# Performance work log

Measured on AMD Instinct MI355X. Metric: run time of the kernel, lower is better.

## Reference

```python
import jax, jax.numpy as jnp
import numpy as np

B, L, H, V = 256, 200, 128, 50000
NLAYER, K = 2, 20
NEG = -1e10


def setup_inputs() -> dict:
    key = jax.random.key(0)
    ks = jax.random.split(key, 14)
    lens = jax.random.randint(ks[0], (B,), 50, L + 1)
    pos = jnp.arange(L)
    valid = pos[None, :] < lens[:, None]                       # [B,L] bool
    seq = jnp.where(valid, jax.random.randint(ks[1], (B, L), 1, V), 0)
    lengths = valid.astype(jnp.int32)                          # >0 where real token
    reverse_lengths = jnp.where(valid, lens[:, None] - pos[None, :], 0)  # 1..len, 0=pad

    def nrm(k, shape, s=0.02):
        return jax.random.normal(k, shape, jnp.float32) * s

    emb_w = nrm(ks[2], (V, H)).at[0].set(0.0)
    wnoise_w = nrm(ks[3], (L + 1, H)).at[0].set(0.0)
    cluster_w = nrm(ks[4], (L + 1, 1)).at[0].set(0.0)
    ffn1_w = nrm(ks[5], (H, H), 0.05)
    ffn1_b = jnp.zeros((H,), jnp.float32)
    ffn2_w = nrm(ks[6], (H, H), 0.05)
    ffn2_b = jnp.zeros((H,), jnp.float32)
    ln_g = jnp.ones((H,), jnp.float32)
    ln_b = jnp.zeros((H,), jnp.float32)
    gate_w = nrm(ks[7], (2 * H, H), 0.05)
    coff = jax.random.normal(ks[8], (NLAYER, B, L, L), jnp.float32)  # fixed noise (torch.normal)
    return dict(seq=seq, lengths=lengths, reverse_lengths=reverse_lengths,
                emb_w=emb_w, wnoise_w=wnoise_w, cluster_w=cluster_w,
                ffn1_w=ffn1_w, ffn1_b=ffn1_b, ffn2_w=ffn2_w, ffn2_b=ffn2_b,
                ln_g=ln_g, ln_b=ln_b, gate_w=gate_w, coff=coff)


def _sp(x):  # torch.nn.Softplus(threshold=1): identity above 1
    return jnp.where(x > 1.0, x, jnp.log1p(jnp.exp(jnp.minimum(x, 1.0))))


def _forward(seq, lengths, reverse_lengths, emb_w, wnoise_w, cluster_w,
             ffn1_w, ffn1_b, ffn2_w, ffn2_b, ln_g, ln_b, gate_w, coff):
    b, l = seq.shape
    mask = (lengths > 0).astype(jnp.float32)                   # [B,L]
    hidden = emb_w[seq]                                        # [B,L,H]
    slen = jnp.sum(mask, axis=1)                               # [B]
    e_s = hidden[jnp.arange(b), (slen - 1).astype(jnp.int32)]  # last real token state
    zero_layer = jnp.sum(hidden, 1) / slen[:, None]
    layer_collect = [zero_layer]
    eye = jnp.eye(l, dtype=hidden.dtype)
    pair_ok = mask[:, :, None] * mask[:, None, :]              # [B,L,L]
    for i in range(coff.shape[0]):
        wn = wnoise_w[reverse_lengths]                         # [B,L,H]
        sim = jnp.einsum('bld,bmd->blm', hidden, hidden)
        nrm = jnp.linalg.norm(hidden, axis=2, keepdims=True)   # [B,L,1]
        sim = sim / (nrm * nrm.transpose(0, 2, 1) + 1e-6)      # cosine similarity
        diag = cluster_w[reverse_lengths][..., 0]              # [B,L]
        sim = sim + diag[:, :, None] * eye                     # diag_embed add
        sim = sim + coff[i] * _sp(jnp.einsum('bld,bmd->blm', hidden, wn))
        msim = jnp.where(pair_ok == 0.0, NEG, sim)             # masked_fill
        _, idx = jax.lax.top_k(msim, K)                        # [B,L,K]
        sel = jnp.zeros_like(msim).at[jnp.arange(b)[:, None, None],
                                      jnp.arange(l)[None, :, None], idx].set(1.0)
        edges = sel * (msim > NEG).astype(msim.dtype)          # top-k & above-threshold
        cluster_label = edges.transpose(0, 2, 1)
        sim_softmax = jax.nn.softmax(msim, axis=2)
        ssm = cluster_label * sim_softmax                      # [B,L,L] sparse-weighted
        update_hidden = jnp.einsum('blm,bmd->bld', ssm, hidden)
        cmask = jnp.sum(ssm, axis=2)                           # [B,L]
        cmask = cmask / jnp.maximum(jnp.linalg.norm(cmask, axis=1, keepdims=True), 1e-12)
        if i > 0:
            update_hidden = update_hidden * (slen > 1.0).astype(hidden.dtype)[:, None, None]
        feed1 = jax.nn.relu(update_hidden @ ffn1_w + ffn1_b)
        pre = feed1 @ ffn2_w + ffn2_b + update_hidden          # dropout = identity (eval)
        mu = jnp.mean(pre, -1, keepdims=True)
        var = jnp.var(pre, -1, keepdims=True)
        feed2 = (pre - mu) / jnp.sqrt(var + 1e-5) * ln_g + ln_b
        layer_collect.append(jnp.sum(feed2 * cmask[:, :, None], 1))
    e_c = jnp.mean(jnp.stack(layer_collect, 1), 1)             # [B,H]
    alpha = jax.nn.sigmoid(jnp.concatenate([e_c, e_s], -1) @ gate_w)
    sess = alpha * e_c + (1.0 - alpha) * e_s
    scores = sess @ emb_w.T                                    # [B,V]
    return scores


def reference(seq, lengths, reverse_lengths, emb_w, wnoise_w, cluster_w,
              ffn1_w, ffn1_b, ffn2_w, ffn2_b, ln_g, ln_b, gate_w, coff):
    scores = _forward(seq, lengths, reverse_lengths, emb_w, wnoise_w, cluster_w,
                      ffn1_w, ffn1_b, ffn2_w, ffn2_b, ln_g, ln_b, gate_w, coff)
    return (scores, jnp.asarray(0.0, jnp.float32))  # con_loss == 0 when abs=True
```

## Files before the change

kernel.cpp:

```cpp
#include <hip/hip_runtime.h>
#include <cstdint>
#include <cstddef>

namespace {
constexpr int B = 256, L = 200, H = 128, V = 50000, TK = 20;
constexpr int NT = 1563;
constexpr float NEGV = -1e10f;
}

using bf16x8 = __attribute__((ext_vector_type(8))) short;
using s16x8  = __attribute__((ext_vector_type(8))) short;
using f32x16 = __attribute__((ext_vector_type(16))) float;

__device__ inline unsigned short f2bf(float f) {
  unsigned int u = __float_as_uint(f);
  unsigned int r = (u + 0x7fffu + ((u >> 16) & 1u)) >> 16;
  return (unsigned short)r;
}

#define DPP_QUAD_XOR1 0xB1
#define DPP_QUAD_XOR2 0x4E
#define DPP_ROW_HMIRR 0x141
#define DPP_ROW_MIRR  0x140

template <int CTRL>
__device__ inline unsigned dpp16_max_step(unsigned v) {
  unsigned t = (unsigned)__builtin_amdgcn_update_dpp(0, (int)v, CTRL, 0xF, 0xF, true);
  return v > t ? v : t;
}
__device__ inline unsigned grp16_max(unsigned v) {
  v = dpp16_max_step<DPP_QUAD_XOR1>(v);
  v = dpp16_max_step<DPP_QUAD_XOR2>(v);
  v = dpp16_max_step<DPP_ROW_HMIRR>(v);
  v = dpp16_max_step<DPP_ROW_MIRR>(v);
  return v;
}
template <int CTRL>
__device__ inline float dpp16_add_step(float v) {
  int t = __builtin_amdgcn_update_dpp(0, __float_as_int(v), CTRL, 0xF, 0xF, true);
  return v + __int_as_float(t);
}
__device__ inline float grp16_sum(float v) {
  v = dpp16_add_step<DPP_QUAD_XOR1>(v);
  v = dpp16_add_step<DPP_QUAD_XOR2>(v);
  v = dpp16_add_step<DPP_ROW_HMIRR>(v);
  v = dpp16_add_step<DPP_ROW_MIRR>(v);
  return v;
}

__device__ inline unsigned f2key(float f) {
  unsigned b = __float_as_uint(f);
  unsigned m = (unsigned)((int)b >> 31);
  return b ^ (m | 0x80000000u);
}
__device__ inline float key2f(unsigned u) {
  unsigned b = (u & 0x80000000u) ? (u & 0x7fffffffu) : ~u;
  return __uint_as_float(b);
}

__global__ __launch_bounds__(256) void k_embed(const int* __restrict__ seq,
                                               const int* __restrict__ rev,
                                               const float* __restrict__ emb,
                                               const float* __restrict__ wnoise,
                                               float* __restrict__ hidden,
                                               float* __restrict__ nrm,
                                               s16x8* __restrict__ hbh,
                                               s16x8* __restrict__ hbl,
                                               s16x8* __restrict__ wnh,
                                               s16x8* __restrict__ wnl) {
  int b = blockIdx.x / 7, lt = blockIdx.x % 7;
  int t = threadIdx.x;
  int r = t >> 3, c2 = t & 7;
  int l = lt * 32 + r;
  bool valid = l < L;
  float vv[16], wv[16];
  if (valid) {
    int row = b * L + l;
    int tok = seq[row];
    const float4* ep = (const float4*)&emb[(size_t)tok * H + c2 * 16];
    const float4* wp = (const float4*)&wnoise[(size_t)rev[row] * H + c2 * 16];
#pragma unroll
    for (int i = 0; i < 4; ++i) {
      float4 x = ep[i];
      vv[i * 4 + 0] = x.x; vv[i * 4 + 1] = x.y; vv[i * 4 + 2] = x.z; vv[i * 4 + 3] = x.w;
      float4 y = wp[i];
      wv[i * 4 + 0] = y.x; wv[i * 4 + 1] = y.y; wv[i * 4 + 2] = y.z; wv[i * 4 + 3] = y.w;
    }
  } else {
#pragma unroll
    for (int i = 0; i < 16; ++i) { vv[i] = 0.f; wv[i] = 0.f; }
  }
  if (valid) {
    int row = b * L + l;
#pragma unroll
    for (int i = 0; i < 4; ++i)
      *(float4*)&hidden[(size_t)row * H + c2 * 16 + i * 4] =
          make_float4(vv[i * 4], vv[i * 4 + 1], vv[i * 4 + 2], vv[i * 4 + 3]);
    float s = 0.f;
#pragma unroll
    for (int i = 0; i < 16; ++i) s += vv[i] * vv[i];
    s += __shfl_down(s, 4, 8);
    s += __shfl_down(s, 2, 8);
    s += __shfl_down(s, 1, 8);
    if (c2 == 0) nrm[row] = sqrtf(s);
  }
  s16x8 h0, h1, l0, l1, w0, w1, x0, x1;
#pragma unroll
  for (int i = 0; i < 8; ++i) {
    unsigned short hi = f2bf(vv[i]);
    h0[i] = (short)hi;
    l0[i] = (short)f2bf(vv[i] - __uint_as_float((unsigned)hi << 16));
    unsigned short wh = f2bf(wv[i]);
    w0[i] = (short)wh;
    x0[i] = (short)f2bf(wv[i] - __uint_as_float((unsigned)wh << 16));
  }
#pragma unroll
  for (int i = 0; i < 8; ++i) {
    unsigned short hi = f2bf(vv[8 + i]);
    h1[i] = (short)hi;
    l1[i] = (short)f2bf(vv[8 + i] - __uint_as_float((unsigned)hi << 16));
    unsigned short wh = f2bf(wv[8 + i]);
    w1[i] = (short)wh;
    x1[i] = (short)f2bf(wv[8 + i] - __uint_as_float((unsigned)wh << 16));
  }
  size_t fi0 = ((size_t)(b * 7 + lt) * 8 + c2) * 64 + r;
  size_t fi1 = fi0 + 32;
  hbh[fi0] = h0; hbh[fi1] = h1;
  hbl[fi0] = l0; hbl[fi1] = l1;
  wnh[fi0] = w0; wnh[fi1] = w1;
  wnl[fi0] = x0; wnl[fi1] = x1;
}

__global__ __launch_bounds__(512) void k_init(const int* __restrict__ lengths,
                                              const float* __restrict__ hidden,
                                              float* __restrict__ ecacc,
                                              float* __restrict__ e_s) {
  int b = blockIdx.x, tid = threadIdx.x;
  __shared__ float part[4][128];
  __shared__ int wcnt[8];
  __shared__ int s_slen;
  int c = (tid < L && lengths[b * L + tid] > 0) ? 1 : 0;
  for (int o = 32; o > 0; o >>= 1) c += __shfl_down(c, o, 64);
  if ((tid & 63) == 0) wcnt[tid >> 6] = c;
  __syncthreads();
  if (tid == 0) {
    int s = 0;
#pragma unroll
    for (int i = 0; i < 8; ++i) s += wcnt[i];
    s_slen = s;
  }
  int h = tid & 127, seg = tid >> 7;
  float s = 0.f;
  for (int l = seg; l < L; l += 4) s += hidden[(size_t)(b * L + l) * H + h];
  part[seg][h] = s;
  __syncthreads();
  if (tid < 128) {
    float tot = part[0][h] + part[1][h] + part[2][h] + part[3][h];
    int slen = s_slen;
    ecacc[b * H + h] = tot / (float)slen;
    e_s[b * H + h] = hidden[(size_t)(b * L + slen - 1) * H + h];
  }
}

__global__ __launch_bounds__(256) void k_simws(const s16x8* __restrict__ hbh,
                                               const s16x8* __restrict__ hbl,
                                               const s16x8* __restrict__ wnh,
                                               const s16x8* __restrict__ wnl,
                                               const float* __restrict__ nrm,
                                               const int* __restrict__ rev,
                                               const float* __restrict__ cluster,
                                               float* __restrict__ S0,
                                               float* __restrict__ WS) {
  int orig = blockIdx.x;
  int xcd = orig & 7, slot = orig >> 3;
  int b = xcd * 32 + slot / 14;
  int rem = slot % 14;
  int lt = rem >> 1, half = rem & 1;
  int wid = threadIdx.x >> 6, lane = threadIdx.x & 63;
  int mt = half * 4 + wid;
  if (mt > 6) return;
  int lr = lane & 31, kh = lane >> 5;
  size_t abase = ((size_t)(b * 7 + lt) * 8) * 64 + lane;
  bf16x8 ah[8], al[8];
#pragma unroll
  for (int ks = 0; ks < 8; ++ks) {
    ah[ks] = (bf16x8)hbh[abase + ks * 64];
    al[ks] = (bf16x8)hbl[abase + ks * 64];
  }
  size_t bbase = ((size_t)(b * 7 + mt) * 8) * 64 + lane;
  f32x16 accs = {}, accw = {};
#pragma unroll
  for (int ks = 0; ks < 8; ++ks) {
    bf16x8 bhh = (bf16x8)hbh[bbase + ks * 64];
    bf16x8 bhl = (bf16x8)hbl[bbase + ks * 64];
    bf16x8 bwh = (bf16x8)wnh[bbase + ks * 64];
    bf16x8 bwl = (bf16x8)wnl[bbase + ks * 64];
    accs = __builtin_amdgcn_mfma_f32_32x32x16_bf16(ah[ks], bhh, accs, 0, 0, 0);
    accs = __builtin_amdgcn_mfma_f32_32x32x16_bf16(ah[ks], bhl, accs, 0, 0, 0);
    accs = __builtin_amdgcn_mfma_f32_32x32x16_bf16(al[ks], bhh, accs, 0, 0, 0);
    accw = __builtin_amdgcn_mfma_f32_32x32x16_bf16(ah[ks], bwh, accw, 0, 0, 0);
    accw = __builtin_amdgcn_mfma_f32_32x32x16_bf16(ah[ks], bwl, accw, 0, 0, 0);
    accw = __builtin_amdgcn_mfma_f32_32x32x16_bf16(al[ks], bwh, accw, 0, 0, 0);
  }
  int m = mt * 32 + lr;
  if (m < L) {
    float nm = nrm[b * L + m];
#pragma unroll
    for (int r = 0; r < 16; ++r) {
      int row = lt * 32 + (r & 3) + 8 * (r >> 2) + 4 * kh;
      if (row < L) {
        float nl = nrm[b * L + row];
        float s0 = accs[r] * __builtin_amdgcn_rcpf(nl * nm + 1e-6f);
        if (row == m) s0 += cluster[rev[b * L + row]];
        size_t o = (size_t)(b * L + row) * L + m;
        S0[o] = s0;
        float x = accw[r];
        WS[o] = (x > 1.f) ? x : __logf(1.f + __expf(x));
      }
    }
  }
}

__global__ __launch_bounds__(256) void k_rowpass(const float* __restrict__ S0,
                                                 const float* __restrict__ WS,
                                                 const float* __restrict__ coff_i,
                                                 const int* __restrict__ lengths,
                                                 float* __restrict__ P,
                                                 unsigned char* __restrict__ ET) {
  int wid = threadIdx.x >> 6, lane = threadIdx.x & 63;
  int g = lane >> 4, q = lane & 15;
  int bb = blockIdx.x / 13, blk = blockIdx.x % 13;
  int l = blk * 16 + wid * 4 + g;
  bool lvalid = l < L;
  int lrow = bb * L + (lvalid ? l : 0);
  bool mask_l = lvalid && (lengths[lrow] > 0);
  size_t base = (size_t)lrow * L;
  float val[13]; unsigned key[13]; unsigned vmask = 0;
#pragma unroll
  for (int j = 0; j < 13; ++j) {
    int m = q + 16 * j;
    float v = 0.f; bool ok = false;
    if (mask_l && m < L) {
      ok = lengths[bb * L + m] > 0;
      if (ok) v = S0[base + m] + coff_i[base + m] * WS[base + m];
    }
    val[j] = v;
    key[j] = ok ? f2key(v) : 0u;
    vmask |= ok ? (1u << j) : 0u;
  }
  unsigned Mu = 0u;
  for (int t = 0; t < TK; ++t) {
    unsigned lv = key[0]; int lj = 0;
#pragma unroll
    for (int j = 1; j < 13; ++j) {
      bool gt = key[j] > lv;
      lv = gt ? key[j] : lv;
      lj = gt ? j : lj;
    }
    unsigned gm = grp16_max(lv);
    if (t == 0) Mu = gm;
    if (__all(gm == 0u)) break;
    unsigned long long bal = __ballot(lv == gm && gm != 0u);
    unsigned long long mine = bal & (0xFFFFull << (g * 16));
    int owner = mine ? (int)__builtin_ctzll(mine) : -1;
    bool is_owner = (lane == owner);
    if (is_owner) {
      int m = q + 16 * lj;
      ET[((size_t)bb * L + m) * L + l] = 1;
    }
#pragma unroll
    for (int j = 0; j < 13; ++j) key[j] = (is_owner && lj == j) ? 0u : key[j];
  }
  float M = key2f(Mu);
  float e[13]; float s = 0.f;
#pragma unroll
  for (int j = 0; j < 13; ++j) {
    float ev = ((vmask >> j) & 1u) ? __expf(val[j] - M) : 0.f;
    e[j] = ev; s += ev;
  }
  s = grp16_sum(s);
  float inv = (s > 0.f) ? __builtin_amdgcn_rcpf(s) : 0.f;
  if (lvalid) {
#pragma unroll
    for (int j = 0; j < 13; ++j) {
      int m = q + 16 * j;
      if (m < L) P[base + m] = e[j] * inv;
    }
  }
}

__global__ __launch_bounds__(256) void k_compact(float* __restrict__ P,
                                                 unsigned char* __restrict__ ET,
                                                 float* __restrict__ cmask,
                                                 int* __restrict__ cnt) {
  int wid = threadIdx.x >> 6, lane = threadIdx.x & 63;
  int row = blockIdx.x * 4 + wid;
  size_t base = (size_t)row * L;
  float w[4];
  float s = 0.f;
#pragma unroll
  for (int j = 0; j < 4; ++j) {
    int m = lane + 64 * j;
    float ww = 0.f;
    if (m < L) ww = P[base + m] * (float)ET[base + m];
    w[j] = ww; s += ww;
  }
  float ssum = s;
  for (int off = 1; off < 64; off <<= 1) ssum += __shfl_xor(ssum, off, 64);
  if (lane == 0) cmask[row] = ssum;
  int pos_base = 0;
#pragma unroll
  for (int j = 0; j < 4; ++j) {
    bool nz = (w[j] != 0.f);
    unsigned long long mk = __ballot(nz);
    int rank = __popcll(mk & ((1ull << lane) - 1ull));
    if (nz) {
      int pos = pos_base + rank;
      ET[base + pos] = (unsigned char)(lane + 64 * j);
      P[base + pos] = w[j];
    }
    pos_base += (int)__popcll(mk);
  }
  if (lane == 0) cnt[row] = pos_base;
}

__global__ __launch_bounds__(64) void k_cnorm(float* __restrict__ cmask) {
  int b = blockIdx.x, lane = threadIdx.x;
  float v[4]; float s = 0.f;
#pragma unroll
  for (int j = 0; j < 4; ++j) {
    int l = lane + 64 * j;
    float x = (l < L) ? cmask[b * L + l] : 0.f;
    v[j] = x; s += x * x;
  }
  for (int off = 1; off < 64; off <<= 1) s += __shfl_xor(s, off, 64);
  float inv = 1.f / fmaxf(sqrtf(s), 1e-12f);
#pragma unroll
  for (int j = 0; j < 4; ++j) {
    int l = lane + 64 * j;
    if (l < L) cmask[b * L + l] = v[j] * inv;
  }
}

__global__ __launch_bounds__(256) void k_update(const float* __restrict__ P,
                                                const unsigned char* __restrict__ ET,
                                                const int* __restrict__ cnt,
                                                const float* __restrict__ hidden,
                                                float* __restrict__ upd) {
  int row = blockIdx.x * 2 + (threadIdx.x >> 7);
  int h = threadIdx.x & 127;
  int b = row / L;
  size_t base = (size_t)row * L;
  int n = cnt[row];
  float acc = 0.f;
  for (int e0 = 0; e0 < n; e0 += TK) {
    float w[TK]; int m[TK];
    float4 p4[5];
#pragma unroll
    for (int i = 0; i < 5; ++i) p4[i] = *(const float4*)&P[base + e0 + i * 4];
#pragma unroll
    for (int i = 0; i < 5; ++i) {
      w[i * 4 + 0] = p4[i].x; w[i * 4 + 1] = p4[i].y;
      w[i * 4 + 2] = p4[i].z; w[i * 4 + 3] = p4[i].w;
    }
#pragma unroll
    for (int e = 0; e < TK; ++e) m[e] = ET[base + e0 + e];
    float hv[TK];
#pragma unroll
    for (int e = 0; e < TK; ++e)
      hv[e] = hidden[(size_t)(b * L + m[e]) * H + h];
#pragma unroll
    for (int e = 0; e < TK; ++e)
      acc += ((e0 + e) < n ? w[e] : 0.f) * hv[e];
  }
  upd[(size_t)row * H + h] = acc;
}

__global__ __launch_bounds__(256) void k_ffn(float* __restrict__ upd,
                                             const float* __restrict__ W1,
                                             const float* __restrict__ b1,
                                             const float* __restrict__ W2,
                                             const float* __restrict__ b2,
                                             const float* __restrict__ g,
                                             const float* __restrict__ beta,
                                             const float* __restrict__ cmask) {
  constexpr int AS = 136;
  __shared__ __align__(16) char smem[4 * 64 * AS * 2];
  short* ahs = (short*)smem;
  short* als = ahs + 64 * AS;
  short* f1h = (short*)(smem + 2 * 64 * AS * 2);
  short* f1l = f1h + 64 * AS;
  float (*ps)[132] = (float (*)[132])smem;
  __shared__ float mus[64], rsd[64];
  int row0 = blockIdx.x * 64;
  int tid = threadIdx.x;
  int wid = tid >> 6, lane = tid & 63;
  int lr = lane & 31, kh = lane >> 5;
  int n0 = wid * 32;
  int n = n0 + lr;
#pragma unroll
  for (int it = 0; it < 8; ++it) {
    int f = it * 256 + tid;
    int r = f >> 5, c4 = (f & 31) * 4;
    float4 v = *(const float4*)&upd[(size_t)(row0 + r) * H + c4];
    float vv[4] = {v.x, v.y, v.z, v.w};
    unsigned short hh[4]; short ll[4];
#pragma unroll
    for (int q2 = 0; q2 < 4; ++q2) {
      hh[q2] = f2bf(vv[q2]);
      ll[q2] = (short)f2bf(vv[q2] - __uint_as_float((unsigned)hh[q2] << 16));
    }
    uint2 ph = make_uint2((unsigned)hh[0] | ((unsigned)hh[1] << 16),
                          (unsigned)hh[2] | ((unsigned)hh[3] << 16));
    uint2 pl = make_uint2((unsigned short)ll[0] | ((unsigned)(unsigned short)ll[1] << 16),
                          (unsigned short)ll[2] | ((unsigned)(unsigned short)ll[3] << 16));
    *(uint2*)&ahs[r * AS + c4] = ph;
    *(uint2*)&als[r * AS + c4] = pl;
  }
  __syncthreads();
  bf16x8 wfh[8], wfl[8];
#pragma unroll
  for (int ks = 0; ks < 8; ++ks) {
#pragma unroll
    for (int i = 0; i < 8; ++i) {
      float w = W1[(size_t)(ks * 16 + kh * 8 + i) * H + n];
      unsigned short hi = f2bf(w);
      wfh[ks][i] = (short)hi;
      wfl[ks][i] = (short)f2bf(w - __uint_as_float((unsigned)hi << 16));
    }
  }
  f32x16 acc0, acc1;
  {
    float bv = b1[n];
#pragma unroll
    for (int r = 0; r < 16; ++r) { acc0[r] = bv; acc1[r] = bv; }
  }
#pragma unroll
  for (int ks = 0; ks < 8; ++ks) {
    bf16x8 xh0 = *(const bf16x8*)&ahs[(0 * 32 + lr) * AS + ks * 16 + kh * 8];
    bf16x8 xl0 = *(const bf16x8*)&als[(0 * 32 + lr) * AS + ks * 16 + kh * 8];
    bf16x8 xh1 = *(const bf16x8*)&ahs[(1 * 32 + lr) * AS + ks * 16 + kh * 8];
    bf16x8 xl1 = *(const bf16x8*)&als[(1 * 32 + lr) * AS + ks * 16 + kh * 8];
    acc0 = __builtin_amdgcn_mfma_f32_32x32x16_bf16(xh0, wfh[ks], acc0, 0, 0, 0);
    acc0 = __builtin_amdgcn_mfma_f32_32x32x16_bf16(xl0, wfh[ks], acc0, 0, 0, 0);
    acc0 = __builtin_amdgcn_mfma_f32_32x32x16_bf16(xh0, wfl[ks], acc0, 0, 0, 0);
    acc1 = __builtin_amdgcn_mfma_f32_32x32x16_bf16(xh1, wfh[ks], acc1, 0, 0, 0);
    acc1 = __builtin_amdgcn_mfma_f32_32x32x16_bf16(xl1, wfh[ks], acc1, 0, 0, 0);
    acc1 = __builtin_amdgcn_mfma_f32_32x32x16_bf16(xh1, wfl[ks], acc1, 0, 0, 0);
  }
#pragma unroll
  for (int r = 0; r < 16; ++r) {
    int crow = (r & 3) + 8 * (r >> 2) + 4 * kh;
    float f0 = fmaxf(acc0[r], 0.f);
    unsigned short h0 = f2bf(f0);
    f1h[crow * AS + n] = (short)h0;
    f1l[crow * AS + n] = (short)f2bf(f0 - __uint_as_float((unsigned)h0 << 16));
    float f1v = fmaxf(acc1[r], 0.f);
    unsigned short h1 = f2bf(f1v);
    f1h[(32 + crow) * AS + n] = (short)h1;
    f1l[(32 + crow) * AS + n] = (short)f2bf(f1v - __uint_as_float((unsigned)h1 << 16));
  }
  __syncthreads();
#pragma unroll
  for (int ks = 0; ks < 8; ++ks) {
#pragma unroll
    for (int i = 0; i < 8; ++i) {
      float w = W2[(size_t)(ks * 16 + kh * 8 + i) * H + n];
      unsigned short hi = f2bf(w);
      wfh[ks][i] = (short)hi;
      wfl[ks][i] = (short)f2bf(w - __uint_as_float((unsigned)hi << 16));
    }
  }
  {
    float bv = b2[n];
#pragma unroll
    for (int r = 0; r < 16; ++r) { acc0[r] = bv; acc1[r] = bv; }
  }
#pragma unroll
  for (int ks = 0; ks < 8; ++ks) {
    bf16x8 xh0 = *(const bf16x8*)&f1h[(0 * 32 + lr) * AS + ks * 16 + kh * 8];
    bf16x8 xl0 = *(const bf16x8*)&f1l[(0 * 32 + lr) * AS + ks * 16 + kh * 8];
    bf16x8 xh1 = *(const bf16x8*)&f1h[(1 * 32 + lr) * AS + ks * 16 + kh * 8];
    bf16x8 xl1 = *(const bf16x8*)&f1l[(1 * 32 + lr) * AS + ks * 16 + kh * 8];
    acc0 = __builtin_amdgcn_mfma_f32_32x32x16_bf16(xh0, wfh[ks], acc0, 0, 0, 0);
    acc0 = __builtin_amdgcn_mfma_f32_32x32x16_bf16(xl0, wfh[ks], acc0, 0, 0, 0);
    acc0 = __builtin_amdgcn_mfma_f32_32x32x16_bf16(xh0, wfl[ks], acc0, 0, 0, 0);
    acc1 = __builtin_amdgcn_mfma_f32_32x32x16_bf16(xh1, wfh[ks], acc1, 0, 0, 0);
    acc1 = __builtin_amdgcn_mfma_f32_32x32x16_bf16(xl1, wfh[ks], acc1, 0, 0, 0);
    acc1 = __builtin_amdgcn_mfma_f32_32x32x16_bf16(xh1, wfl[ks], acc1, 0, 0, 0);
  }
#pragma unroll
  for (int r = 0; r < 16; ++r) {
    int crow = (r & 3) + 8 * (r >> 2) + 4 * kh;
    float p0 = acc0[r] + upd[(size_t)(row0 + crow) * H + n];
    float p1 = acc1[r] + upd[(size_t)(row0 + 32 + crow) * H + n];
    acc0[r] = p0; acc1[r] = p1;
    ps[crow][n] = p0;
    ps[32 + crow][n] = p1;
  }
  __syncthreads();
  {
    int r = tid >> 2, sub = tid & 3;
    float s = 0.f, sq = 0.f;
#pragma unroll
    for (int j = 0; j < 8; ++j) {
      float4 x = *(const float4*)&ps[r][sub * 32 + j * 4];
      s += x.x + x.y + x.z + x.w;
      sq += x.x * x.x + x.y * x.y + x.z * x.z + x.w * x.w;
    }
    s += __shfl_down(s, 2, 4);  s += __shfl_down(s, 1, 4);
    sq += __shfl_down(sq, 2, 4); sq += __shfl_down(sq, 1, 4);
    if (sub == 0) {
      float mu = s * (1.f / 128.f);
      float var = sq * (1.f / 128.f) - mu * mu;
      mus[r] = mu;
      rsd[r] = rsqrtf(var + 1e-5f);
    }
  }
  __syncthreads();
  {
    float gn = g[n], bn = beta[n];
#pragma unroll
    for (int r = 0; r < 16; ++r) {
      int crow = (r & 3) + 8 * (r >> 2) + 4 * kh;
      float o0 = ((acc0[r] - mus[crow]) * rsd[crow] * gn + bn) * cmask[row0 + crow];
      float o1 = ((acc1[r] - mus[32 + crow]) * rsd[32 + crow] * gn + bn) * cmask[row0 + 32 + crow];
      upd[(size_t)(row0 + crow) * H + n] = o0;
      upd[(size_t)(row0 + 32 + crow) * H + n] = o1;
    }
  }
}

__global__ __launch_bounds__(512) void k_ecadd(const float* __restrict__ wf,
                                               float* __restrict__ ecacc) {
  int b = blockIdx.x, tid = threadIdx.x;
  __shared__ float part[4][128];
  int h = tid & 127, seg = tid >> 7;
  float s = 0.f;
  for (int l = seg; l < L; l += 4) s += wf[(size_t)(b * L + l) * H + h];
  part[seg][h] = s;
  __syncthreads();
  if (tid < 128)
    ecacc[b * H + h] += part[0][h] + part[1][h] + part[2][h] + part[3][h];
}

__global__ __launch_bounds__(256) void k_embconv(const float* __restrict__ emb,
                                                 s16x8* __restrict__ ebh,
                                                 s16x8* __restrict__ ebl) {
  int nt = blockIdx.x;
  int t = threadIdx.x;
  int r = t >> 3, c2 = t & 7;
  int n = nt * 32 + r;
  float vv[16];
  if (n < V) {
    const float4* ep = (const float4*)&emb[(size_t)n * H + c2 * 16];
#pragma unroll
    for (int i = 0; i < 4; ++i) {
      float4 x = ep[i];
      vv[i * 4 + 0] = x.x; vv[i * 4 + 1] = x.y; vv[i * 4 + 2] = x.z; vv[i * 4 + 3] = x.w;
    }
  } else {
#pragma unroll
    for (int i = 0; i < 16; ++i) vv[i] = 0.f;
  }
  s16x8 h0, h1, l0, l1;
#pragma unroll
  for (int i = 0; i < 8; ++i) {
    unsigned short hi = f2bf(vv[i]);
    h0[i] = (short)hi;
    l0[i] = (short)f2bf(vv[i] - __uint_as_float((unsigned)hi << 16));
    unsigned short hj = f2bf(vv[8 + i]);
    h1[i] = (short)hj;
    l1[i] = (short)f2bf(vv[8 + i] - __uint_as_float((unsigned)hj << 16));
  }
  size_t fi0 = ((size_t)nt * 8 + c2) * 64 + r;
  size_t fi1 = fi0 + 32;
  ebh[fi0] = h0; ebh[fi1] = h1;
  ebl[fi0] = l0; ebl[fi1] = l1;
}

__global__ __launch_bounds__(128) void k_gate(const float* __restrict__ ecacc,
                                              const float* __restrict__ e_s,
                                              const float* __restrict__ gw,
                                              float* __restrict__ sess,
                                              float* __restrict__ out) {
  __shared__ float cat[256];
  int b = blockIdx.x, h = threadIdx.x;
  float ec = ecacc[b * H + h] * (1.f / 3.f);
  float es = e_s[b * H + h];
  cat[h] = ec; cat[128 + h] = es;
  __syncthreads();
  float a = 0.f;
  for (int j = 0; j < 256; ++j) a = fmaf(cat[j], gw[(size_t)j * H + h], a);
  a = 1.f / (1.f + __expf(-a));
  sess[b * H + h] = a * ec + (1.f - a) * es;
  if (b == 0 && h == 0) out[(size_t)B * V] = 0.f;
}

__global__ __launch_bounds__(256) void k_scores(const float* __restrict__ sess,
                                                const s16x8* __restrict__ ebh,
                                                const s16x8* __restrict__ ebl,
                                                float* __restrict__ out) {
  int wid = threadIdx.x >> 6, lane = threadIdx.x & 63;
  int lr = lane & 31, kh = lane >> 5;
  int mt = blockIdx.y;
  int m = mt * 32 + lr;
  bf16x8 ah[8], al[8];
#pragma unroll
  for (int ks = 0; ks < 8; ++ks) {
    const float* sp = &sess[(size_t)m * H + ks * 16 + kh * 8];
    float4 a = *(const float4*)sp;
    float4 c = *(const float4*)(sp + 4);
    float av[8] = {a.x, a.y, a.z, a.w, c.x, c.y, c.z, c.w};
#pragma unroll
    for (int i = 0; i < 8; ++i) {
      unsigned short hi = f2bf(av[i]);
      ah[ks][i] = (short)hi;
      al[ks][i] = (short)f2bf(av[i] - __uint_as_float((unsigned)hi << 16));
    }
  }
  int ntEnd = min(blockIdx.x * 16 + 16, NT);
  for (int nt = blockIdx.x * 16 + wid; nt < ntEnd; nt += 4) {
    size_t bbase = ((size_t)nt * 8) * 64 + lane;
    f32x16 acc = {};
#pragma unroll
    for (int ks = 0; ks < 8; ++ks) {
      bf16x8 bh = (bf16x8)ebh[bbase + ks * 64];
      bf16x8 bl = (bf16x8)ebl[bbase + ks * 64];
      acc = __builtin_amdgcn_mfma_f32_32x32x16_bf16(ah[ks], bh, acc, 0, 0, 0);
      acc = __builtin_amdgcn_mfma_f32_32x32x16_bf16(al[ks], bh, acc, 0, 0, 0);
      acc = __builtin_amdgcn_mfma_f32_32x32x16_bf16(ah[ks], bl, acc, 0, 0, 0);
    }
    int n = nt * 32 + lr;
    if (n < V) {
#pragma unroll
      for (int r = 0; r < 16; ++r) {
        int row = mt * 32 + (r & 3) + 8 * (r >> 2) + 4 * kh;
        out[(size_t)row * V + n] = acc[r];
      }
    }
  }
}

extern "C" void kernel_launch(void* const* d_in, const int* in_sizes, int n_in,
                              void* d_out, int out_size, void* d_ws, size_t ws_size,
                              hipStream_t stream) {
  const int*   seq  = (const int*)d_in[0];
  const int*   lens = (const int*)d_in[1];
  const int*   rev  = (const int*)d_in[2];
  const float* emb  = (const float*)d_in[3];
  const float* wnz  = (const float*)d_in[4];
  const float* clw  = (const float*)d_in[5];
  const float* w1   = (const float*)d_in[6];
  const float* fb1  = (const float*)d_in[7];
  const float* w2   = (const float*)d_in[8];
  const float* fb2  = (const float*)d_in[9];
  const float* lng  = (const float*)d_in[10];
  const float* lnb  = (const float*)d_in[11];
  const float* gw   = (const float*)d_in[12];
  const float* coff = (const float*)d_in[13];
  float* out = (float*)d_out;

  char* ws = (char*)d_ws;
  size_t off = 0;
  auto alloc = [&](size_t bytes) {
    void* p = ws + off;
    off += (bytes + 255) & ~(size_t)255;
    return p;
  };
  float* hidden = (float*)alloc((size_t)B * L * H * 4);
  float* nrm    = (float*)alloc((size_t)B * L * 4);
  float* S0     = (float*)alloc((size_t)B * L * L * 4);
  float* WS     = (float*)alloc((size_t)B * L * L * 4);
  float* P      = (float*)alloc((size_t)B * L * L * 4);
  float* upd    = (float*)alloc((size_t)B * L * H * 4);
  float* cmask  = (float*)alloc((size_t)B * L * 4);
  int*   cnt    = (int*)alloc((size_t)B * L * 4);
  float* e_s    = (float*)alloc((size_t)B * H * 4);
  float* ecacc  = (float*)alloc((size_t)B * H * 4);
  float* sess   = (float*)alloc((size_t)B * H * 4);
  unsigned char* ET = (unsigned char*)alloc((size_t)B * L * L);
  s16x8* hbh = (s16x8*)alloc((size_t)B * 7 * 8 * 64 * 16);
  s16x8* wnh = (s16x8*)alloc((size_t)B * 7 * 8 * 64 * 16);
  s16x8* hbl = (s16x8*)P;
  s16x8* wnl = (s16x8*)upd;
  s16x8* ebh = (s16x8*)S0;
  s16x8* ebl = (s16x8*)WS;

  k_embed<<<B * 7, 256, 0, stream>>>(seq, rev, emb, wnz, hidden, nrm,
                                     hbh, hbl, wnh, wnl);
  k_init<<<B, 512, 0, stream>>>(lens, hidden, ecacc, e_s);
  k_simws<<<B * 14, 256, 0, stream>>>(hbh, hbl, wnh, wnl, nrm, rev, clw, S0, WS);

  for (int i = 0; i < 2; ++i) {
    hipMemsetAsync(ET, 0, (size_t)B * L * L, stream);
    k_rowpass<<<B * 13, 256, 0, stream>>>(S0, WS, coff + (size_t)i * B * L * L,
                                          lens, P, ET);
    k_compact<<<B * L / 4, 256, 0, stream>>>(P, ET, cmask, cnt);
    k_cnorm<<<B, 64, 0, stream>>>(cmask);
    k_update<<<B * L / 2, 256, 0, stream>>>(P, ET, cnt, hidden, upd);
    k_ffn<<<B * L / 64, 256, 0, stream>>>(upd, w1, fb1, w2, fb2, lng, lnb, cmask);
    k_ecadd<<<B, 512, 0, stream>>>(upd, ecacc);
  }

  k_embconv<<<NT, 256, 0, stream>>>(emb, ebh, ebl);
  k_gate<<<B, 128, 0, stream>>>(ecacc, e_s, gw, sess, out);
  k_scores<<<dim3((NT + 15) / 16, 8), 256, 0, stream>>>(sess, ebh, ebl, out);
}
```

Baseline: 460.0 us.

## Fuse compact and update into a gather kernel; two rows per group in rowpass top-k

The row-pass kernel now handles two query rows per 16-lane group. It keeps a running top-3 per lane plus an LDS copy of the keys, so most top-k iterations no longer rescan all 13 registers. The separate compact and update kernels are merged into one k_gather kernel. It compacts the selected weights and indices into shared memory and then gathers hidden rows, which avoids writing and re-reading the compacted P and ET arrays and saves a launch. The cost is more LDS use in rowpass (27 words per thread), and the two-row layout roughly halves the grid size.

```diff
diff --git a/kernel.cpp b/kernel.cpp
--- a/kernel.cpp
+++ b/kernel.cpp
@@ -227,101 +227,179 @@
                                                  const int* __restrict__ lengths,
                                                  float* __restrict__ P,
                                                  unsigned char* __restrict__ ET) {
+  __shared__ unsigned klds[256 * 27];
   int wid = threadIdx.x >> 6, lane = threadIdx.x & 63;
   int g = lane >> 4, q = lane & 15;
-  int bb = blockIdx.x / 13, blk = blockIdx.x % 13;
-  int l = blk * 16 + wid * 4 + g;
-  bool lvalid = l < L;
-  int lrow = bb * L + (lvalid ? l : 0);
-  bool mask_l = lvalid && (lengths[lrow] > 0);
-  size_t base = (size_t)lrow * L;
-  float val[13]; unsigned key[13]; unsigned vmask = 0;
+  int bb = blockIdx.x / 7, blk = blockIdx.x % 7;
+  int g16 = wid * 4 + g;
+  int lA = blk * 32 + g16 * 2, lB = lA + 1;
+  bool lvA = lA < L, lvB = lB < L;
+  int lrowA = bb * L + (lvA ? lA : 0);
+  int lrowB = bb * L + (lvB ? lB : 0);
+  bool mA = lvA && (lengths[lrowA] > 0);
+  bool mB = lvB && (lengths[lrowB] > 0);
+  size_t baseA = (size_t)lrowA * L, baseB = (size_t)lrowB * L;
+  int kbA = threadIdx.x * 27, kbB = kbA + 13;
+  float valA[13], valB[13]; unsigned vmA = 0, vmB = 0;
+  unsigned a0 = 0, a1 = 0, a2 = 0; int aj0 = 0, aj1 = 0, aj2 = 0;
+  unsigned c0 = 0, c1 = 0, c2 = 0; int cj0 = 0, cj1 = 0, cj2 = 0;
 #pragma unroll
   for (int j = 0; j < 13; ++j) {
     int m = q + 16 * j;
-    float v = 0.f; bool ok = false;
-    if (mask_l && m < L) {
-      ok = lengths[bb * L + m] > 0;
-      if (ok) v = S0[base + m] + coff_i[base + m] * WS[base + m];
-    }
-    val[j] = v;
-    key[j] = ok ? f2key(v) : 0u;
-    vmask |= ok ? (1u << j) : 0u;
-  }
-  unsigned Mu = 0u;
+    bool colOk = (m < L) && (lengths[bb * L + m] > 0);
+    bool okA = mA && colOk, okB = mB && colOk;
+    float vA = 0.f, vB = 0.f;
+    if (okA) vA = S0[baseA + m] + coff_i[baseA + m] * WS[baseA + m];
+    if (okB) vB = S0[baseB + m] + coff_i[baseB + m] * WS[baseB + m];
+    valA[j] = vA; valB[j] = vB;
+    unsigned kA = okA ? f2key(vA) : 0u;
+    unsigned kB = okB ? f2key(vB) : 0u;
+    vmA |= okA ? (1u << j) : 0u;
+    vmB |= okB ? (1u << j) : 0u;
+    klds[kbA + j] = kA;
+    klds[kbB + j] = kB;
+    if (kA > a0)      { a2 = a1; aj2 = aj1; a1 = a0; aj1 = aj0; a0 = kA; aj0 = j; }
+    else if (kA > a1) { a2 = a1; aj2 = aj1; a1 = kA; aj1 = j; }
+    else if (kA > a2) { a2 = kA; aj2 = j; }
+    if (kB > c0)      { c2 = c1; cj2 = cj1; c1 = c0; cj1 = cj0; c0 = kB; cj0 = j; }
+    else if (kB > c1) { c2 = c1; cj2 = cj1; c1 = kB; cj1 = j; }
+    else if (kB > c2) { c2 = kB; cj2 = j; }
+  }
+  unsigned ccA = a0; int cjA = aj0; int consA = 0;
+  unsigned ccB = c0; int cjB = cj0; int consB = 0;
+  unsigned MuA = 0u, MuB = 0u;
   for (int t = 0; t < TK; ++t) {
-    unsigned lv = key[0]; int lj = 0;
-#pragma unroll
-    for (int j = 1; j < 13; ++j) {
-      bool gt = key[j] > lv;
-      lv = gt ? key[j] : lv;
-      lj = gt ? j : lj;
-    }
-    unsigned gm = grp16_max(lv);
-    if (t == 0) Mu = gm;
-    if (__all(gm == 0u)) break;
-    unsigned long long bal = __ballot(lv == gm && gm != 0u);
-    unsigned long long mine = bal & (0xFFFFull << (g * 16));
-    int owner = mine ? (int)__builtin_ctzll(mine) : -1;
-    bool is_owner = (lane == owner);
-    if (is_owner) {
-      int m = q + 16 * lj;
-      ET[((size_t)bb * L + m) * L + l] = 1;
-    }
-#pragma unroll
-    for (int j = 0; j < 13; ++j) key[j] = (is_owner && lj == j) ? 0u : key[j];
-  }
-  float M = key2f(Mu);
-  float e[13]; float s = 0.f;
+    unsigned gmA = grp16_max(ccA);
+    unsigned gmB = grp16_max(ccB);
+    if (t == 0) { MuA = gmA; MuB = gmB; }
+    if (__all((gmA | gmB) == 0u)) break;
+    unsigned long long balA = __ballot(ccA == gmA && gmA != 0u);
+    unsigned long long balB = __ballot(ccB == gmB && gmB != 0u);
+    unsigned long long grpm = 0xFFFFull << (g * 16);
+    unsigned long long mineA = balA & grpm;
+    unsigned long long mineB = balB & grpm;
+    int ownA = mineA ? (int)__builtin_ctzll(mineA) : -1;
+    int ownB = mineB ? (int)__builtin_ctzll(mineB) : -1;
+    if (lane == ownA) {
+      int m = q + 16 * cjA;
+      ET[((size_t)bb * L + m) * L + lA] = 1;
+      klds[kbA + cjA] = 0u;
+      ++consA;
+      if (consA == 1)      { ccA = a1; cjA = aj1; }
+      else if (consA == 2) { ccA = a2; cjA = aj2; }
+      else {
+        unsigned x = 0; int xj = 0;
+#pragma unroll
+        for (int j = 0; j < 13; ++j) {
+          unsigned k2 = klds[kbA + j];
+          if (k2 > x) { x = k2; xj = j; }
+        }
+        ccA = x; cjA = xj;
+      }
+    }
+    if (lane == ownB) {
+      int m = q + 16 * cjB;
+      ET[((size_t)bb * L + m) * L + lB] = 1;
+      klds[kbB + cjB] = 0u;
+      ++consB;
+      if (consB == 1)      { ccB = c1; cjB = cj1; }
+      else if (consB == 2) { ccB = c2; cjB = cj2; }
+      else {
+        unsigned x = 0; int xj = 0;
+#pragma unroll
+        for (int j = 0; j < 13; ++j) {
+          unsigned k2 = klds[kbB + j];
+          if (k2 > x) { x = k2; xj = j; }
+        }
+        ccB = x; cjB = xj;
+      }
+    }
+  }
+  float MA = key2f(MuA), MB = key2f(MuB);
+  float eA[13], eB[13]; float sA = 0.f, sB = 0.f;
 #pragma unroll
   for (int j = 0; j < 13; ++j) {
-    float ev = ((vmask >> j) & 1u) ? __expf(val[j] - M) : 0.f;
-    e[j] = ev; s += ev;
-  }
-  s = grp16_sum(s);
-  float inv = (s > 0.f) ? __builtin_amdgcn_rcpf(s) : 0.f;
-  if (lvalid) {
-#pragma unroll
-    for (int j = 0; j < 13; ++j) {
-      int m = q + 16 * j;
-      if (m < L) P[base + m] = e[j] * inv;
-    }
-  }
-}
-
-__global__ __launch_bounds__(256) void k_compact(float* __restrict__ P,
-                                                 unsigned char* __restrict__ ET,
-                                                 float* __restrict__ cmask,
-                                                 int* __restrict__ cnt) {
-  int wid = threadIdx.x >> 6, lane = threadIdx.x & 63;
-  int row = blockIdx.x * 4 + wid;
-  size_t base = (size_t)row * L;
-  float w[4];
-  float s = 0.f;
-#pragma unroll
-  for (int j = 0; j < 4; ++j) {
-    int m = lane + 64 * j;
-    float ww = 0.f;
-    if (m < L) ww = P[base + m] * (float)ET[base + m];
-    w[j] = ww; s += ww;
-  }
-  float ssum = s;
-  for (int off = 1; off < 64; off <<= 1) ssum += __shfl_xor(ssum, off, 64);
-  if (lane == 0) cmask[row] = ssum;
-  int pos_base = 0;
-#pragma unroll
-  for (int j = 0; j < 4; ++j) {
-    bool nz = (w[j] != 0.f);
-    unsigned long long mk = __ballot(nz);
-    int rank = __popcll(mk & ((1ull << lane) - 1ull));
-    if (nz) {
-      int pos = pos_base + rank;
-      ET[base + pos] = (unsigned char)(lane + 64 * j);
-      P[base + pos] = w[j];
-    }
-    pos_base += (int)__popcll(mk);
-  }
-  if (lane == 0) cnt[row] = pos_base;
+    float evA = ((vmA >> j) & 1u) ? __expf(valA[j] - MA) : 0.f;
+    float evB = ((vmB >> j) & 1u) ? __expf(valB[j] - MB) : 0.f;
+    eA[j] = evA; sA += evA;
+    eB[j] = evB; sB += evB;
+  }
+  sA = grp16_sum(sA);
+  sB = grp16_sum(sB);
+  float invA = (sA > 0.f) ? __builtin_amdgcn_rcpf(sA) : 0.f;
+  float invB = (sB > 0.f) ? __builtin_amdgcn_rcpf(sB) : 0.f;
+#pragma unroll
+  for (int j = 0; j < 13; ++j) {
+    int m = q + 16 * j;
+    if (m < L) {
+      if (lvA) P[baseA + m] = eA[j] * invA;
+      if (lvB) P[baseB + m] = eB[j] * invB;
+    }
+  }
+}
+
+__global__ __launch_bounds__(512) void k_gather(const float* __restrict__ P,
+                                                const unsigned char* __restrict__ ET,
+                                                const float* __restrict__ hidden,
+                                                float* __restrict__ cmask,
+                                                float* __restrict__ upd) {
+  __shared__ float wls[4][224];
+  __shared__ unsigned char ils[4][224];
+  __shared__ int s_cnt[4];
+  int wv = threadIdx.x >> 6, lane = threadIdx.x & 63;
+  if (wv < 4) {
+    int rowW = blockIdx.x * 4 + wv;
+    size_t baseW = (size_t)rowW * L;
+    float w[4]; float s = 0.f;
+#pragma unroll
+    for (int j = 0; j < 4; ++j) {
+      int m = lane + 64 * j;
+      float ww = 0.f;
+      if (m < L) ww = P[baseW + m] * (float)ET[baseW + m];
+      w[j] = ww; s += ww;
+    }
+    float ssum = s;
+    for (int off = 1; off < 64; off <<= 1) ssum += __shfl_xor(ssum, off, 64);
+    if (lane == 0) cmask[rowW] = ssum;
+    int pos_base = 0;
+#pragma unroll
+    for (int j = 0; j < 4; ++j) {
+      bool nz = (w[j] != 0.f);
+      unsigned long long mk = __ballot(nz);
+      int rank = __popcll(mk & ((1ull << lane) - 1ull));
+      if (nz) {
+        int pos = pos_base + rank;
+        ils[wv][pos] = (unsigned char)(lane + 64 * j);
+        wls[wv][pos] = w[j];
+      }
+      pos_base += (int)__popcll(mk);
+    }
+    if (lane == 0) s_cnt[wv] = pos_base;
+    int padEnd = ((pos_base + TK - 1) / TK) * TK;
+    for (int p = pos_base + lane; p < padEnd; p += 64) {
+      ils[wv][p] = 0; wls[wv][p] = 0.f;
+    }
+  }
+  __syncthreads();
+  int half = threadIdx.x >> 7;
+  int h = threadIdx.x & 127;
+  int row = blockIdx.x * 4 + half;
+  int b = row / L;
+  int n = s_cnt[half];
+  float acc = 0.f;
+  for (int e0 = 0; e0 < n; e0 += TK) {
+    float w[TK]; int m[TK];
+#pragma unroll
+    for (int e = 0; e < TK; ++e) { w[e] = wls[half][e0 + e]; m[e] = ils[half][e0 + e]; }
+    float hv[TK];
+#pragma unroll
+    for (int e = 0; e < TK; ++e)
+      hv[e] = hidden[(size_t)(b * L + m[e]) * H + h];
+#pragma unroll
+    for (int e = 0; e < TK; ++e)
+      acc += w[e] * hv[e];
+  }
+  upd[(size_t)row * H + h] = acc;
 }
 
 __global__ __launch_bounds__(64) void k_cnorm(float* __restrict__ cmask) {
@@ -340,40 +418,6 @@
     int l = lane + 64 * j;
     if (l < L) cmask[b * L + l] = v[j] * inv;
   }
-}
-
-__global__ __launch_bounds__(256) void k_update(const float* __restrict__ P,
-                                                const unsigned char* __restrict__ ET,
-                                                const int* __restrict__ cnt,
-                                                const float* __restrict__ hidden,
-                                                float* __restrict__ upd) {
-  int row = blockIdx.x * 2 + (threadIdx.x >> 7);
-  int h = threadIdx.x & 127;
-  int b = row / L;
-  size_t base = (size_t)row * L;
-  int n = cnt[row];
-  float acc = 0.f;
-  for (int e0 = 0; e0 < n; e0 += TK) {
-    float w[TK]; int m[TK];
-    float4 p4[5];
-#pragma unroll
-    for (int i = 0; i < 5; ++i) p4[i] = *(const float4*)&P[base + e0 + i * 4];
-#pragma unroll
-    for (int i = 0; i < 5; ++i) {
-      w[i * 4 + 0] = p4[i].x; w[i * 4 + 1] = p4[i].y;
-      w[i * 4 + 2] = p4[i].z; w[i * 4 + 3] = p4[i].w;
-    }
-#pragma unroll
-    for (int e = 0; e < TK; ++e) m[e] = ET[base + e0 + e];
-    float hv[TK];
-#pragma unroll
-    for (int e = 0; e < TK; ++e)
-      hv[e] = hidden[(size_t)(b * L + m[e]) * H + h];
-#pragma unroll
-    for (int e = 0; e < TK; ++e)
-      acc += ((e0 + e) < n ? w[e] : 0.f) * hv[e];
-  }
-  upd[(size_t)row * H + h] = acc;
 }
 
 __global__ __launch_bounds__(256) void k_ffn(float* __restrict__ upd,
@@ -694,11 +738,10 @@
 
   for (int i = 0; i < 2; ++i) {
     hipMemsetAsync(ET, 0, (size_t)B * L * L, stream);
-    k_rowpass<<<B * 13, 256, 0, stream>>>(S0, WS, coff + (size_t)i * B * L * L,
-                                          lens, P, ET);
-    k_compact<<<B * L / 4, 256, 0, stream>>>(P, ET, cmask, cnt);
+    k_rowpass<<<B * 7, 256, 0, stream>>>(S0, WS, coff + (size_t)i * B * L * L,
+                                         lens, P, ET);
+    k_gather<<<B * L / 4, 512, 0, stream>>>(P, ET, hidden, cmask, upd);
     k_cnorm<<<B, 64, 0, stream>>>(cmask);
-    k_update<<<B * L / 2, 256, 0, stream>>>(P, ET, cnt, hidden, upd);
     k_ffn<<<B * L / 64, 256, 0, stream>>>(upd, w1, fb1, w2, fb2, lng, lnb, cmask);
     k_ecadd<<<B, 512, 0, stream>>>(upd, ecacc);
   }
```

Result: no change. 463.4 us (+0.8%).
